# Performance work log

Measured on AMD Instinct MI355X. Metric: run time of the kernel, lower is better.

The kernel has to match this reference:

```python
import jax, jax.numpy as jnp
import numpy as np

HEAD_SIZE = 64

def setup_inputs() -> dict:
    key = jax.random.key(0)
    k1, k2, k3, k4 = jax.random.split(key, 4)
    x = jax.random.normal(k1, (4, 4096, 1024), dtype=jnp.float32)
    scale = 1.0 / np.sqrt(1024)
    Wk = jax.random.normal(k2, (1024, HEAD_SIZE), dtype=jnp.float32) * scale
    Wq = jax.random.normal(k3, (1024, HEAD_SIZE), dtype=jnp.float32) * scale
    Wv = jax.random.normal(k4, (1024, HEAD_SIZE), dtype=jnp.float32) * scale
    return {"x": x, "Wk": Wk, "Wq": Wq, "Wv": Wv}

def reference(x, Wk, Wq, Wv):
    # x: [b, s, d]; W*: [d, h]
    keys = jnp.einsum('bsd,dh->bsh', x, Wk)
    queries = jnp.einsum('bsd,dh->bsh', x, Wq)
    values = jnp.einsum('bsd,dh->bsh', x, Wv)
    scores = jnp.einsum('bqh,bkh->bqk', queries, keys) / jnp.sqrt(
        jnp.asarray(HEAD_SIZE, dtype=jnp.float32))
    attn = jax.nn.softmax(scores, axis=-1)
    return jnp.einsum('bqk,bkh->bqh', attn, values)
```

## Files before the change

### kernel.cpp

```cpp
#include <hip/hip_runtime.h>
#include <stdint.h>

typedef short bf16x8 __attribute__((ext_vector_type(8)));
typedef __fp16 f16x2 __attribute__((ext_vector_type(2)));
typedef __fp16 f16x4 __attribute__((ext_vector_type(4)));
typedef float f32x4 __attribute__((ext_vector_type(4)));
typedef unsigned short u16;

static __device__ __forceinline__ f32x4 mfma_bf16_k32(bf16x8 a, bf16x8 b, f32x4 c) {
  return __builtin_amdgcn_mfma_f32_16x16x32_bf16(a, b, c, 0, 0, 0);
}
static __device__ __forceinline__ f32x4 mfma_f16_k16(f16x4 a, f16x4 b, f32x4 c) {
  return __builtin_amdgcn_mfma_f32_16x16x16f16(a, b, c, 0, 0, 0);
}

static __device__ __forceinline__ float fast_exp2(float x) {
#if __has_builtin(__builtin_amdgcn_exp2f)
  return __builtin_amdgcn_exp2f(x);
#else
  return exp2f(x);
#endif
}

static __device__ __forceinline__ u16 f2bf(float f) {
  union { float f; uint32_t u; } v; v.f = f;
  uint32_t u = v.u;
  u += 0x7FFFu + ((u >> 16) & 1u);
  return (u16)(u >> 16);
}

static __device__ __forceinline__ int lds_off(int row, int col) {
  return row * 128 + (col ^ ((row & 7) << 4));
}

__global__ __launch_bounds__(256) void prep_wt(const float* __restrict__ Wk,
                                               const float* __restrict__ Wq,
                                               const float* __restrict__ Wv,
                                               u16* __restrict__ WTp) {
  int idx = blockIdx.x * 256 + threadIdx.x;
  if (idx >= 24576) return;
  const int lane = idx & 63, kc = (idx >> 6) & 31, nt = idx >> 11;
  const int l15 = lane & 15, g = lane >> 4;
  int n = nt * 16 + l15;
  const int k0 = kc * 32 + 8 * g;
  const float* W;
  float scale = 1.0f;
  if (n < 64)        { W = Wq; scale = 0.125f * 1.44269504088896f; }
  else if (n < 128)  { W = Wk; n -= 64; }
  else               { W = Wv; n -= 128; }
  union { u16 s[8]; bf16x8 v; } cv;
#pragma unroll
  for (int j = 0; j < 8; ++j) cv.s[j] = f2bf(W[(k0 + j) * 64 + n] * scale);
  *(bf16x8*)(WTp + (size_t)idx * 8) = cv.v;
}

__global__ __launch_bounds__(256) void qkv_proj(const float* __restrict__ x,
                                                const u16* __restrict__ WTp,
                                                u16* __restrict__ Q,
                                                u16* __restrict__ K,
                                                __fp16* __restrict__ VT) {
  __shared__ __align__(16) char xs[32768];
  const int lane = threadIdx.x & 63;
  const int wv   = threadIdx.x >> 6;
  const int l15  = lane & 15, g = lane >> 4;
  const long r0  = (long)blockIdx.x * 16;

#pragma unroll
  for (int rr = 0; rr < 4; ++rr) {
    const int row = wv * 4 + rr;
    const float* xp = x + (r0 + row) * 1024;
#pragma unroll
    for (int ii = 0; ii < 4; ++ii) {
      float4 f = *(const float4*)(xp + ii * 256 + lane * 4);
      union { u16 s[4]; uint2 u; } cv;
      cv.s[0] = f2bf(f.x); cv.s[1] = f2bf(f.y);
      cv.s[2] = f2bf(f.z); cv.s[3] = f2bf(f.w);
      int off = row * 2048 + ii * 512 + lane * 8;
      off ^= (row & 7) << 4;
      *(uint2*)&xs[off] = cv.u;
    }
  }
  __syncthreads();

  f32x4 acc[3];
#pragma unroll
  for (int j = 0; j < 3; ++j) acc[j] = (f32x4){0.f, 0.f, 0.f, 0.f};

  const u16* wbase = WTp + (size_t)(3 * wv) * 16384 + lane * 8;

#pragma unroll 8
  for (int kc = 0; kc < 32; ++kc) {
    int aoff = l15 * 2048 + kc * 64 + g * 16;
    aoff ^= (l15 & 7) << 4;
    bf16x8 af = *(const bf16x8*)&xs[aoff];
#pragma unroll
    for (int j = 0; j < 3; ++j) {
      bf16x8 bf = *(const bf16x8*)(wbase + (size_t)j * 16384 + kc * 512);
      acc[j] = mfma_bf16_k32(af, bf, acc[j]);
    }
  }

  const int b = (int)(r0 >> 12), sb = (int)(r0 & 4095);
#pragma unroll
  for (int j = 0; j < 3; ++j) {
    const int n = 3 * wv + j;
    f32x4 r = acc[j];
    if (n < 4) {
#pragma unroll
      for (int i = 0; i < 4; ++i)
        Q[(r0 + 4 * g + i) * 64 + n * 16 + l15] = f2bf(r[i]);
    } else if (n < 8) {
#pragma unroll
      for (int i = 0; i < 4; ++i)
        K[(r0 + 4 * g + i) * 64 + (n - 4) * 16 + l15] = f2bf(r[i]);
    } else {
      union { f16x2 h[2]; uint2 u; } vv;
      vv.h[0] = __builtin_amdgcn_cvt_pkrtz(r[0], r[1]);
      vv.h[1] = __builtin_amdgcn_cvt_pkrtz(r[2], r[3]);
      *(uint2*)(VT + (long)b * 262144 + ((n - 8) * 16 + l15) * 4096 + sb + 4 * g) = vv.u;
    }
  }
}

__global__ __launch_bounds__(512, 4) void flash_attn(const u16* __restrict__ Q,
                                                     const u16* __restrict__ K,
                                                     const __fp16* __restrict__ VT,
                                                     float* __restrict__ out,
                                                     float* __restrict__ po,
                                                     float* __restrict__ pl,
                                                     int niter, int direct) {
  __shared__ __align__(16) char kv_lds[2][2][8192];
  const int lane = threadIdx.x & 63, wv = threadIdx.x >> 6;
  const int l15 = lane & 15, g = lane >> 4;
  const int tile = (int)blockIdx.x & 127;
  const int c = (int)blockIdx.x >> 7;
  const int b = tile >> 5;
  const int r = (tile & 31) * 128 + wv * 16;
  const long qglob = (long)b * 4096 + r;
  const int t0 = c * niter;

  const char* Kb = (const char*)(K  + (long)b * 262144);
  const char* Vb = (const char*)(VT + (long)b * 262144);

  bf16x8 qf[2];
#pragma unroll
  for (int h = 0; h < 2; ++h)
    qf[h] = *(const bf16x8*)(Q + (qglob + l15) * 64 + 32 * h + 8 * g);

  f32x4 o[4];
#pragma unroll
  for (int n = 0; n < 4; ++n) o[n] = (f32x4){0.f, 0.f, 0.f, 0.f};
  f32x4 lacc = (f32x4){0.f, 0.f, 0.f, 0.f};
  const f32x4 zero4 = (f32x4){0.f, 0.f, 0.f, 0.f};
  const f16x4 one4 = {(__fp16)1.f, (__fp16)1.f, (__fp16)1.f, (__fp16)1.f};

  uint4 sd[2];
  auto stage_load = [&](int t) {
#pragma unroll
    for (int jj = 0; jj < 2; ++jj) {
      const int j = wv * 2 + jj;
      const int d = (j & 7) * 1024 + lane * 16;
      const char* src;
      if (j < 8) src = Kb + (long)t * 8192 + d;
      else       src = Vb + (long)(d >> 7) * 8192 + (long)t * 128 + (d & 127);
      sd[jj] = *(const uint4*)src;
    }
  };
  auto stage_write = [&](int buf) {
#pragma unroll
    for (int jj = 0; jj < 2; ++jj) {
      const int j = wv * 2 + jj;
      const int d = (j & 7) * 1024 + lane * 16;
      const int off = d ^ (((d >> 7) & 7) << 4);
      *(uint4*)&kv_lds[buf][j < 8 ? 0 : 1][off] = sd[jj];
    }
  };

  auto body = [&](int cb, int t, bool stage) {
    if (stage) stage_load(t + 1);

    bf16x8 kf[4][2];
#pragma unroll
    for (int tt = 0; tt < 4; ++tt)
#pragma unroll
      for (int h = 0; h < 2; ++h)
        kf[tt][h] = *(const bf16x8*)&kv_lds[cb][0][lds_off(tt * 16 + l15, 64 * h + 16 * g)];
    f16x4 vf[4][4];
#pragma unroll
    for (int n = 0; n < 4; ++n)
#pragma unroll
      for (int tt = 0; tt < 4; ++tt)
        vf[n][tt] = *(const f16x4*)&kv_lds[cb][1][lds_off(16 * n + l15, 32 * tt + 8 * g)];

    f32x4 st[4];
#pragma unroll
    for (int tt = 0; tt < 4; ++tt) {
      st[tt] = mfma_bf16_k32(kf[tt][0], qf[0], zero4);
      st[tt] = mfma_bf16_k32(kf[tt][1], qf[1], st[tt]);
    }
#pragma unroll
    for (int tt = 0; tt < 4; ++tt)
#pragma unroll
      for (int i = 0; i < 4; ++i) st[tt][i] = fast_exp2(st[tt][i]);
    f16x4 pb[4];
#pragma unroll
    for (int tt = 0; tt < 4; ++tt) {
      union { f16x2 h[2]; f16x4 v; } u;
      u.h[0] = __builtin_amdgcn_cvt_pkrtz(st[tt][0], st[tt][1]);
      u.h[1] = __builtin_amdgcn_cvt_pkrtz(st[tt][2], st[tt][3]);
      pb[tt] = u.v;
    }

#pragma unroll
    for (int tt = 0; tt < 4; ++tt)
      lacc = mfma_f16_k16(one4, pb[tt], lacc);
#pragma unroll
    for (int tt = 0; tt < 4; ++tt)
#pragma unroll
      for (int n = 0; n < 4; ++n)
        o[n] = mfma_f16_k16(vf[n][tt], pb[tt], o[n]);

    if (stage) stage_write(cb ^ 1);
    __syncthreads();
  };

  stage_load(t0);
  stage_write(0);
  __syncthreads();

  for (int it = 0; it + 2 < niter; it += 2) {
    body(0, t0 + it, true);
    body(1, t0 + it + 1, true);
  }
  body(0, t0 + niter - 2, true);
  body(1, t0 + niter - 1, false);

  const float lsum = lacc[0];
  if (direct) {
    float linv = 1.f / lsum;
#pragma unroll
    for (int n = 0; n < 4; ++n) {
      float4 v = {o[n][0] * linv, o[n][1] * linv, o[n][2] * linv, o[n][3] * linv};
      *(float4*)(out + (qglob + l15) * 64 + n * 16 + 4 * g) = v;
    }
  } else {
    const long pr = (long)c * 16384 + qglob + l15;
#pragma unroll
    for (int n = 0; n < 4; ++n) {
      float4 v = {o[n][0], o[n][1], o[n][2], o[n][3]};
      *(float4*)(po + pr * 64 + n * 16 + 4 * g) = v;
    }
    if (g == 0) pl[pr] = lsum;
  }
}

__global__ __launch_bounds__(256) void combine(const float* __restrict__ po,
                                               const float* __restrict__ pl,
                                               float* __restrict__ out, int nspl) {
  const int r = blockIdx.x * 4 + (threadIdx.x >> 6);
  const int h = threadIdx.x & 63;
  float L = 0.f, acc = 0.f;
  for (int c = 0; c < nspl; ++c) {
    L += pl[c * 16384 + r];
    acc += po[((long)c * 16384 + r) * 64 + h];
  }
  out[(long)r * 64 + h] = acc / L;
}

extern "C" void kernel_launch(void* const* d_in, const int* in_sizes, int n_in,
                              void* d_out, int out_size, void* d_ws, size_t ws_size,
                              hipStream_t stream) {
  const float* x  = (const float*)d_in[0];
  const float* Wk = (const float*)d_in[1];
  const float* Wq = (const float*)d_in[2];
  const float* Wv = (const float*)d_in[3];
  float* out = (float*)d_out;

  char* ws = (char*)d_ws;
  u16* WTp    = (u16*)ws;
  u16* Q      = (u16*)(ws + 393216);
  u16* K      = (u16*)(ws + 393216 + 2097152);
  __fp16* VT  = (__fp16*)(ws + 393216 + 2 * 2097152);
  const size_t base = 393216 + 3 * 2097152;
  const size_t per  = (size_t)16384 * 64 * 4 + (size_t)16384 * 4;

  int nspl, direct;
  if (ws_size >= base + 8 * per)      { nspl = 8; direct = 0; }
  else if (ws_size >= base + 4 * per) { nspl = 4; direct = 0; }
  else if (ws_size >= base + 2 * per) { nspl = 2; direct = 0; }
  else                                { nspl = 1; direct = 1; }

  float* po = (float*)(ws + base);
  float* pl = po + (size_t)nspl * 16384 * 64;

  prep_wt<<<96, 256, 0, stream>>>(Wk, Wq, Wv, WTp);
  qkv_proj<<<1024, 256, 0, stream>>>(x, WTp, Q, K, VT);
  flash_attn<<<128 * nspl, 512, 0, stream>>>(Q, K, VT, out, po, pl, 64 / nspl, direct);
  if (!direct) combine<<<4096, 256, 0, stream>>>(po, pl, out, nspl);
}
```

Before: 82.04 us.

## Process two query tiles per wave to reuse K/V fragments; store fp16 partials

Each wave now handles 32 query rows (two 16-row tiles), so every K and V fragment read from LDS feeds twice as many MFMAs, and each block covers 256 rows with half as many blocks. The row sum is now accumulated with VALU adds plus cross-lane shuffles instead of the ones-vector MFMA. Split partial outputs are stored as fp16, halving the partial-result traffic to and from the combine kernel. The costs are more registers per wave, fewer blocks in the grid (lower parallelism), and some precision loss in the stored partials.

```diff
diff --git a/kernel.cpp b/kernel.cpp
--- a/kernel.cpp
+++ b/kernel.cpp
@@ -126,33 +126,36 @@
                                                      const u16* __restrict__ K,
                                                      const __fp16* __restrict__ VT,
                                                      float* __restrict__ out,
-                                                     float* __restrict__ po,
+                                                     __fp16* __restrict__ po,
                                                      float* __restrict__ pl,
                                                      int niter, int direct) {
   __shared__ __align__(16) char kv_lds[2][2][8192];
   const int lane = threadIdx.x & 63, wv = threadIdx.x >> 6;
   const int l15 = lane & 15, g = lane >> 4;
-  const int tile = (int)blockIdx.x & 127;
-  const int c = (int)blockIdx.x >> 7;
-  const int b = tile >> 5;
-  const int r = (tile & 31) * 128 + wv * 16;
+  const int tile = (int)blockIdx.x & 63;
+  const int c = (int)blockIdx.x >> 6;
+  const int b = tile >> 4;
+  const int r = (tile & 15) * 256 + wv * 32;
   const long qglob = (long)b * 4096 + r;
   const int t0 = c * niter;
 
   const char* Kb = (const char*)(K  + (long)b * 262144);
   const char* Vb = (const char*)(VT + (long)b * 262144);
 
-  bf16x8 qf[2];
-#pragma unroll
-  for (int h = 0; h < 2; ++h)
-    qf[h] = *(const bf16x8*)(Q + (qglob + l15) * 64 + 32 * h + 8 * g);
-
-  f32x4 o[4];
-#pragma unroll
-  for (int n = 0; n < 4; ++n) o[n] = (f32x4){0.f, 0.f, 0.f, 0.f};
-  f32x4 lacc = (f32x4){0.f, 0.f, 0.f, 0.f};
+  bf16x8 qf[2][2];
+#pragma unroll
+  for (int p = 0; p < 2; ++p)
+#pragma unroll
+    for (int h = 0; h < 2; ++h)
+      qf[p][h] = *(const bf16x8*)(Q + (qglob + p * 16 + l15) * 64 + 32 * h + 8 * g);
+
+  f32x4 o[4][2];
+#pragma unroll
+  for (int n = 0; n < 4; ++n)
+#pragma unroll
+    for (int p = 0; p < 2; ++p) o[n][p] = (f32x4){0.f, 0.f, 0.f, 0.f};
+  float lsum[2] = {0.f, 0.f};
   const f32x4 zero4 = (f32x4){0.f, 0.f, 0.f, 0.f};
-  const f16x4 one4 = {(__fp16)1.f, (__fp16)1.f, (__fp16)1.f, (__fp16)1.f};
 
   uint4 sd[2];
   auto stage_load = [&](int t) {
@@ -179,46 +182,54 @@
   auto body = [&](int cb, int t, bool stage) {
     if (stage) stage_load(t + 1);
 
-    bf16x8 kf[4][2];
-#pragma unroll
-    for (int tt = 0; tt < 4; ++tt)
-#pragma unroll
-      for (int h = 0; h < 2; ++h)
-        kf[tt][h] = *(const bf16x8*)&kv_lds[cb][0][lds_off(tt * 16 + l15, 64 * h + 16 * g)];
-    f16x4 vf[4][4];
-#pragma unroll
-    for (int n = 0; n < 4; ++n)
+    f16x4 pb[2][4];
+    {
+      bf16x8 kf[4][2];
 #pragma unroll
       for (int tt = 0; tt < 4; ++tt)
-        vf[n][tt] = *(const f16x4*)&kv_lds[cb][1][lds_off(16 * n + l15, 32 * tt + 8 * g)];
-
-    f32x4 st[4];
-#pragma unroll
-    for (int tt = 0; tt < 4; ++tt) {
-      st[tt] = mfma_bf16_k32(kf[tt][0], qf[0], zero4);
-      st[tt] = mfma_bf16_k32(kf[tt][1], qf[1], st[tt]);
-    }
-#pragma unroll
-    for (int tt = 0; tt < 4; ++tt)
-#pragma unroll
-      for (int i = 0; i < 4; ++i) st[tt][i] = fast_exp2(st[tt][i]);
-    f16x4 pb[4];
-#pragma unroll
-    for (int tt = 0; tt < 4; ++tt) {
-      union { f16x2 h[2]; f16x4 v; } u;
-      u.h[0] = __builtin_amdgcn_cvt_pkrtz(st[tt][0], st[tt][1]);
-      u.h[1] = __builtin_amdgcn_cvt_pkrtz(st[tt][2], st[tt][3]);
-      pb[tt] = u.v;
-    }
-
-#pragma unroll
-    for (int tt = 0; tt < 4; ++tt)
-      lacc = mfma_f16_k16(one4, pb[tt], lacc);
-#pragma unroll
-    for (int tt = 0; tt < 4; ++tt)
-#pragma unroll
-      for (int n = 0; n < 4; ++n)
-        o[n] = mfma_f16_k16(vf[n][tt], pb[tt], o[n]);
+#pragma unroll
+        for (int h = 0; h < 2; ++h)
+          kf[tt][h] = *(const bf16x8*)&kv_lds[cb][0][lds_off(tt * 16 + l15, 64 * h + 16 * g)];
+#pragma unroll
+      for (int p = 0; p < 2; ++p) {
+        f32x4 st[4];
+#pragma unroll
+        for (int tt = 0; tt < 4; ++tt) {
+          st[tt] = mfma_bf16_k32(kf[tt][0], qf[p][0], zero4);
+          st[tt] = mfma_bf16_k32(kf[tt][1], qf[p][1], st[tt]);
+        }
+#pragma unroll
+        for (int tt = 0; tt < 4; ++tt)
+#pragma unroll
+          for (int i = 0; i < 4; ++i) st[tt][i] = fast_exp2(st[tt][i]);
+        float rsum = 0.f;
+#pragma unroll
+        for (int tt = 0; tt < 4; ++tt)
+#pragma unroll
+          for (int i = 0; i < 4; ++i) rsum += st[tt][i];
+        lsum[p] += rsum;
+#pragma unroll
+        for (int tt = 0; tt < 4; ++tt) {
+          union { f16x2 h[2]; f16x4 v; } u;
+          u.h[0] = __builtin_amdgcn_cvt_pkrtz(st[tt][0], st[tt][1]);
+          u.h[1] = __builtin_amdgcn_cvt_pkrtz(st[tt][2], st[tt][3]);
+          pb[p][tt] = u.v;
+        }
+      }
+    }
+
+#pragma unroll
+    for (int n = 0; n < 4; ++n) {
+      f16x4 vfn[4];
+#pragma unroll
+      for (int tt = 0; tt < 4; ++tt)
+        vfn[tt] = *(const f16x4*)&kv_lds[cb][1][lds_off(16 * n + l15, 32 * tt + 8 * g)];
+#pragma unroll
+      for (int tt = 0; tt < 4; ++tt) {
+        o[n][0] = mfma_f16_k16(vfn[tt], pb[0][tt], o[n][0]);
+        o[n][1] = mfma_f16_k16(vfn[tt], pb[1][tt], o[n][1]);
+      }
+    }
 
     if (stage) stage_write(cb ^ 1);
     __syncthreads();
@@ -235,26 +246,33 @@
   body(0, t0 + niter - 2, true);
   body(1, t0 + niter - 1, false);
 
-  const float lsum = lacc[0];
-  if (direct) {
-    float linv = 1.f / lsum;
-#pragma unroll
-    for (int n = 0; n < 4; ++n) {
-      float4 v = {o[n][0] * linv, o[n][1] * linv, o[n][2] * linv, o[n][3] * linv};
-      *(float4*)(out + (qglob + l15) * 64 + n * 16 + 4 * g) = v;
-    }
-  } else {
-    const long pr = (long)c * 16384 + qglob + l15;
-#pragma unroll
-    for (int n = 0; n < 4; ++n) {
-      float4 v = {o[n][0], o[n][1], o[n][2], o[n][3]};
-      *(float4*)(po + pr * 64 + n * 16 + 4 * g) = v;
-    }
-    if (g == 0) pl[pr] = lsum;
-  }
-}
-
-__global__ __launch_bounds__(256) void combine(const float* __restrict__ po,
+#pragma unroll
+  for (int p = 0; p < 2; ++p) {
+    float ls = lsum[p];
+    ls += __shfl_xor(ls, 16);
+    ls += __shfl_xor(ls, 32);
+    if (direct) {
+      float linv = 1.f / ls;
+#pragma unroll
+      for (int n = 0; n < 4; ++n) {
+        float4 v = {o[n][p][0] * linv, o[n][p][1] * linv, o[n][p][2] * linv, o[n][p][3] * linv};
+        *(float4*)(out + (qglob + p * 16 + l15) * 64 + n * 16 + 4 * g) = v;
+      }
+    } else {
+      const long pr = (long)c * 16384 + qglob + p * 16 + l15;
+#pragma unroll
+      for (int n = 0; n < 4; ++n) {
+        union { f16x2 h[2]; uint2 u; } vv;
+        vv.h[0] = __builtin_amdgcn_cvt_pkrtz(o[n][p][0], o[n][p][1]);
+        vv.h[1] = __builtin_amdgcn_cvt_pkrtz(o[n][p][2], o[n][p][3]);
+        *(uint2*)(po + pr * 64 + n * 16 + 4 * g) = vv.u;
+      }
+      if (g == 0) pl[pr] = ls;
+    }
+  }
+}
+
+__global__ __launch_bounds__(256) void combine(const __fp16* __restrict__ po,
                                                const float* __restrict__ pl,
                                                float* __restrict__ out, int nspl) {
   const int r = blockIdx.x * 4 + (threadIdx.x >> 6);
@@ -262,7 +280,7 @@
   float L = 0.f, acc = 0.f;
   for (int c = 0; c < nspl; ++c) {
     L += pl[c * 16384 + r];
-    acc += po[((long)c * 16384 + r) * 64 + h];
+    acc += (float)po[((long)c * 16384 + r) * 64 + h];
   }
   out[(long)r * 64 + h] = acc / L;
 }
@@ -282,7 +300,7 @@
   u16* K      = (u16*)(ws + 393216 + 2097152);
   __fp16* VT  = (__fp16*)(ws + 393216 + 2 * 2097152);
   const size_t base = 393216 + 3 * 2097152;
-  const size_t per  = (size_t)16384 * 64 * 4 + (size_t)16384 * 4;
+  const size_t per  = (size_t)16384 * 64 * 2 + (size_t)16384 * 4;
 
   int nspl, direct;
   if (ws_size >= base + 8 * per)      { nspl = 8; direct = 0; }
@@ -290,11 +308,11 @@
   else if (ws_size >= base + 2 * per) { nspl = 2; direct = 0; }
   else                                { nspl = 1; direct = 1; }
 
-  float* po = (float*)(ws + base);
-  float* pl = po + (size_t)nspl * 16384 * 64;
+  __fp16* po = (__fp16*)(ws + base);
+  float*  pl = (float*)(ws + base + (size_t)nspl * 16384 * 64 * 2);
 
   prep_wt<<<96, 256, 0, stream>>>(Wk, Wq, Wv, WTp);
   qkv_proj<<<1024, 256, 0, stream>>>(x, WTp, Q, K, VT);
-  flash_attn<<<128 * nspl, 512, 0, stream>>>(Q, K, VT, out, po, pl, 64 / nspl, direct);
+  flash_attn<<<64 * nspl, 512, 0, stream>>>(Q, K, VT, out, po, pl, 64 / nspl, direct);
   if (!direct) combine<<<4096, 256, 0, stream>>>(po, pl, out, nspl);
 }
```

Result: slower. 96.88 us (+18.1%).
